# Optimization experiments

Hardware: AMD Instinct MI355X
Metric: run time of the kernel (lower is better)

Reference implementation:

```python
import jax, jax.numpy as jnp
import numpy as np

D_MODEL = 1024
NHEAD = 16
DHEAD = D_MODEL // NHEAD
DFF = 4096
B, S = 2, 2048
R = 25                # local_attention_radius = 5*5
K = 5                 # rel_pos_max_distance
W = 2 * R + 1         # window width
EPS = 1e-5


def setup_inputs() -> dict:
    key = jax.random.key(0)
    ks = jax.random.split(key, 12)
    s = 0.02
    g = lambda k, shape: jax.random.normal(k, shape, jnp.float32) * s
    return {
        "src": jax.random.normal(ks[0], (B, S, D_MODEL), jnp.float32),
        # attention in/out projections (W stored [out,in], applied x @ W.T + b)
        "wq": g(ks[1], (D_MODEL, D_MODEL)), "bq": jnp.zeros((D_MODEL,), jnp.float32),
        "wk": g(ks[2], (D_MODEL, D_MODEL)), "bk": jnp.zeros((D_MODEL,), jnp.float32),
        "wv": g(ks[3], (D_MODEL, D_MODEL)), "bv": jnp.zeros((D_MODEL,), jnp.float32),
        "wo": g(ks[4], (D_MODEL, D_MODEL)), "bo": jnp.zeros((D_MODEL,), jnp.float32),
        # relative position embeddings, ids clipped to [-K, K] -> 2K+1 rows
        "rel_emb": g(ks[5], (2 * K + 1, DHEAD)),
        # FFN
        "w1": g(ks[6], (DFF, D_MODEL)), "b1": jnp.zeros((DFF,), jnp.float32),
        "w2": g(ks[7], (D_MODEL, DFF)), "b2": jnp.zeros((D_MODEL,), jnp.float32),
        # layernorms
        "g1": jnp.ones((D_MODEL,), jnp.float32), "beta1": jnp.zeros((D_MODEL,), jnp.float32),
        "g2": jnp.ones((D_MODEL,), jnp.float32), "beta2": jnp.zeros((D_MODEL,), jnp.float32),
    }


def _layernorm(x, g, b):
    m = x.mean(-1, keepdims=True)
    v = ((x - m) ** 2).mean(-1, keepdims=True)
    return (x - m) * jax.lax.rsqrt(v + EPS) * g + b


def _rel_window_attention(x, wq, bq, wk, bk, wv, bv, wo, bo, rel_emb):
    b, s, d = x.shape

    def proj(w, bias):
        return (x @ w.T + bias).reshape(b, s, NHEAD, DHEAD).transpose(0, 2, 1, 3)

    q = proj(wq, bq)  # [B,H,S,Dh]
    k = proj(wk, bk)
    v = proj(wv, bv)

    offsets = jnp.arange(-R, R + 1)                     # [W]
    j = jnp.arange(s)[:, None] + offsets[None, :]       # [S,W] absolute key index
    valid = (j >= 0) & (j < s)
    jc = jnp.clip(j, 0, s - 1)

    scale = 1.0 / np.sqrt(DHEAD).astype(np.float32)
    k_win = k[:, :, jc]                                 # [B,H,S,W,Dh] banded gather
    scores = jnp.einsum('bhsd,bhswd->bhsw', q, k_win) * scale
    rel_ids = jnp.clip(offsets, -K, K) + K              # [W]
    scores = scores + jnp.einsum('bhsd,wd->bhsw', q, rel_emb[rel_ids]) * scale
    scores = jnp.where(valid[None, None], scores, jnp.float32(-1e30))
    attn = jax.nn.softmax(scores, axis=-1)              # [B,H,S,W]

    v_win = v[:, :, jc]                                 # [B,H,S,W,Dh]
    out = jnp.einsum('bhsw,bhswd->bhsd', attn, v_win)
    out = out.transpose(0, 2, 1, 3).reshape(b, s, d)
    return out @ wo.T + bo


def reference(src, wq, bq, wk, bk, wv, bv, wo, bo, rel_emb,
              w1, b1, w2, b2, g1, beta1, g2, beta2):
    # post-norm (norm_first=False default) transformer block, dropout=0 (eval)
    z = _rel_window_attention(src, wq, bq, wk, bk, wv, bv, wo, bo, rel_emb)
    x = _layernorm(src + z, g1, beta1)
    ff = jax.nn.relu(x @ w1.T + b1) @ w2.T + b2
    return _layernorm(x + ff, g2, beta2)
```

## Files before the change

### kernel.cpp

```cpp
#include <hip/hip_runtime.h>


#define D_MODEL 1024
#define SEQ     2048
#define NROWS   4096
#define WIN     51
#define RAD     25

typedef __attribute__((ext_vector_type(8))) __bf16 bf16x8;
typedef __attribute__((ext_vector_type(4))) float  floatx4;

__device__ __forceinline__ unsigned short f2bf(float x) {
    unsigned u = __float_as_uint(x);
    unsigned r = u + 0x7fffu + ((u >> 16) & 1u);
    return (unsigned short)(r >> 16);
}
__device__ __forceinline__ float bf2f(unsigned short h) {
    return __uint_as_float(((unsigned)h) << 16);
}

__device__ __forceinline__ void gld16(const unsigned short* g, unsigned short* l) {
    __builtin_amdgcn_global_load_lds(
        (const __attribute__((address_space(1))) unsigned int*)g,
        (__attribute__((address_space(3))) unsigned int*)l,
        16, 0, 0);
}

__device__ __forceinline__ void cvtgrp(const float* __restrict__ in,
                                       unsigned short* __restrict__ out, int g) {
    float4 f = ((const float4*)in)[g];
    ushort4 u;
    u.x = f2bf(f.x); u.y = f2bf(f.y); u.z = f2bf(f.z); u.w = f2bf(f.w);
    ((ushort4*)out)[g] = u;
}

__global__ __launch_bounds__(256)
void cvt1(const float* __restrict__ src,
          const float* __restrict__ wq, const float* __restrict__ wk,
          const float* __restrict__ wv,
          const float* __restrict__ bq, const float* __restrict__ bk,
          const float* __restrict__ bv,
          unsigned short* __restrict__ xb,
          unsigned short* __restrict__ wqkvb,
          float* __restrict__ bqkv)
{
    int g = blockIdx.x * 256 + threadIdx.x;
    if (g >= 1835200) return;
    if (g < 1048576) { cvtgrp(src, xb, g); return; }
    g -= 1048576;
    if (g < 262144) { cvtgrp(wq, wqkvb, g); return; }
    g -= 262144;
    if (g < 262144) { cvtgrp(wk, wqkvb + 1048576, g); return; }
    g -= 262144;
    if (g < 262144) { cvtgrp(wv, wqkvb + 2097152, g); return; }
    g -= 262144;
    float4 f = (g < 64) ? ((const float4*)bq)[g]
             : (g < 128) ? ((const float4*)bk)[g - 64]
                         : ((const float4*)bv)[g - 128];
    ((float4*)bqkv)[g] = f;
}

__global__ __launch_bounds__(256, 2)
void qkv_cvt(const unsigned short* __restrict__ A,
             const unsigned short* __restrict__ Wt,
             const float* __restrict__ bias,
             unsigned short* __restrict__ Cb,
             const float* __restrict__ wo, const float* __restrict__ w1,
             const float* __restrict__ w2,
             unsigned short* __restrict__ wob,
             unsigned short* __restrict__ w1b,
             unsigned short* __restrict__ w2b)
{
    __shared__ __attribute__((aligned(16))) unsigned short AS[3 * 8192];
    __shared__ __attribute__((aligned(16))) unsigned short BS[3 * 4096];

    if (blockIdx.x >= 384) {
        int g = (blockIdx.x - 384) * 256 + threadIdx.x;
        if (g < 262144) { cvtgrp(wo, wob, g); return; }
        g -= 262144;
        if (g < 1048576) { cvtgrp(w1, w1b, g); return; }
        g -= 1048576;
        cvtgrp(w2, w2b, g);
        return;
    }

    const int t0 = blockIdx.x;
    const int sid = (t0 & 7) * 48 + (t0 >> 3);
    const int bm = (sid / 24) * 256;
    const int bn = (sid % 24) * 128;

    const int tid  = threadIdx.x;
    const int lane = tid & 63;
    const int wave = tid >> 6;
    const int wr   = wave >> 1;
    const int wc   = wave & 1;
    const int fm   = lane & 15;
    const int fq   = lane >> 4;

    const int NT = 32;

    const int ks  = (tid >> 3) & 7;
    const int gi  = tid ^ ks;
    const int r0s = gi >> 2;
    const int c2s = gi & 3;
    const unsigned short* Agp = A  + (size_t)(bm + r0s) * 1024 + c2s * 8;
    const unsigned short* Wgp = Wt + (size_t)(bn + r0s) * 1024 + c2s * 8;
    const size_t istep = (size_t)64 * 1024;

    const int rA  = wr * 128 + fm;
    const int rB  = wc * 64  + fm;
    const int c0A = ((((rA << 2) | fq) ^ (fm >> 1)) << 3);
    const int c0B = ((((rB << 2) | fq) ^ (fm >> 1)) << 3);

    {
        const unsigned short* Ap = Agp;
        const unsigned short* Wp = Wgp;
        gld16(Ap,             AS + tid * 8);
        gld16(Ap + istep,     AS + tid * 8 + 2048);
        gld16(Ap + 2 * istep, AS + tid * 8 + 4096);
        gld16(Ap + 3 * istep, AS + tid * 8 + 6144);
        gld16(Wp,             BS + tid * 8);
        gld16(Wp + istep,     BS + tid * 8 + 2048);
        Ap += 32; Wp += 32;
        gld16(Ap,             AS + 8192 + tid * 8);
        gld16(Ap + istep,     AS + 8192 + tid * 8 + 2048);
        gld16(Ap + 2 * istep, AS + 8192 + tid * 8 + 4096);
        gld16(Ap + 3 * istep, AS + 8192 + tid * 8 + 6144);
        gld16(Wp,             BS + 4096 + tid * 8);
        gld16(Wp + istep,     BS + 4096 + tid * 8 + 2048);
    }
    asm volatile("s_waitcnt vmcnt(6)" ::: "memory");
    __builtin_amdgcn_sched_barrier(0);
    __builtin_amdgcn_s_barrier();
    __builtin_amdgcn_sched_barrier(0);

    floatx4 acc[8][4] = {};
    const unsigned short* Aga = Agp + 64;
    const unsigned short* Wga = Wgp + 64;
    int cbA = 0, cbB = 0;
    int pbA = 16384, pbB = 8192;

    for (int t = 0; t < NT; t++) {
        const bool pf = (t + 2 < NT);

        bf16x8 af[8], bf[4];
        #pragma unroll
        for (int mi = 0; mi < 8; mi++)
            af[mi] = *(const bf16x8*)(AS + cbA + c0A + mi * 512);
        #pragma unroll
        for (int ni = 0; ni < 4; ni++)
            bf[ni] = *(const bf16x8*)(BS + cbB + c0B + ni * 512);

        if (pf) {
            gld16(Aga,             AS + pbA + tid * 8);
            gld16(Aga + istep,     AS + pbA + tid * 8 + 2048);
            gld16(Aga + 2 * istep, AS + pbA + tid * 8 + 4096);
            gld16(Aga + 3 * istep, AS + pbA + tid * 8 + 6144);
            gld16(Wga,             BS + pbB + tid * 8);
            gld16(Wga + istep,     BS + pbB + tid * 8 + 2048);
        }

        __builtin_amdgcn_s_setprio(1);
        #pragma unroll
        for (int mi = 0; mi < 8; mi++)
            #pragma unroll
            for (int ni = 0; ni < 4; ni++)
                acc[mi][ni] = __builtin_amdgcn_mfma_f32_16x16x32_bf16(
                    af[mi], bf[ni], acc[mi][ni], 0, 0, 0);
        __builtin_amdgcn_s_setprio(0);

        if (t + 1 < NT) {
            if (pf) asm volatile("s_waitcnt vmcnt(6)" ::: "memory");
            else    asm volatile("s_waitcnt vmcnt(0)" ::: "memory");
            __builtin_amdgcn_sched_barrier(0);
            __builtin_amdgcn_s_barrier();
            __builtin_amdgcn_sched_barrier(0);
        }
        cbA = (cbA == 16384) ? 0 : cbA + 8192;
        cbB = (cbB == 8192)  ? 0 : cbB + 4096;
        pbA = (pbA == 16384) ? 0 : pbA + 8192;
        pbB = (pbB == 8192)  ? 0 : pbB + 4096;
        Aga += 32;
        Wga += 32;
    }

    const int r0  = bm + wr * 128 + fq * 4;
    const int c0e = bn + wc * 64 + fm;
    #pragma unroll
    for (int mi = 0; mi < 8; mi++) {
        #pragma unroll
        for (int ni = 0; ni < 4; ni++) {
            const int col = c0e + ni * 16;
            const float bv = bias[col];
            #pragma unroll
            for (int rr = 0; rr < 4; rr++) {
                const int row = r0 + mi * 16 + rr;
                Co_store: ;
                float v = acc[mi][ni][rr] + bv;
                Cb[(size_t)row * 3072 + col] = f2bf(v);
            }
        }
    }
}

__global__ __launch_bounds__(512, 2)
void gemm8p(const unsigned short* __restrict__ A,
            const unsigned short* __restrict__ Wt,
            const float* __restrict__ bias,
            unsigned short* __restrict__ Cb,
            int kstride, int kloop, int T, int tncnt,
            int ldc, int relu, size_t sstep1, size_t sstep2)
{
    __shared__ __attribute__((aligned(16))) unsigned short AS[2 * 16384];
    __shared__ __attribute__((aligned(16))) unsigned short BS[2 * 16384];

    const int id = blockIdx.x;
    const int sl = id / T;
    const int t0 = id - sl * T;
    const int sid = (t0 & 7) * (T >> 3) + (t0 >> 3);
    const int bm = (sid / tncnt) * 256;
    const int bn = (sid % tncnt) * 256;

    const int tid  = threadIdx.x;
    const int lane = tid & 63;
    const int wave = tid >> 6;
    const int wr   = wave >> 2;
    const int wc   = wave & 3;
    const int fm   = lane & 15;
    const int fq   = lane >> 4;

    const int kofs  = sl * kloop;
    const int NITER = kloop >> 7;

    const int srow = tid >> 3;
    const int scol = ((tid & 7) ^ ((tid >> 3) & 7)) * 8;
    const unsigned short* PA = A  + (size_t)(bm + srow) * kstride + kofs + scol;
    const unsigned short* PW = Wt + (size_t)(bn + srow) * kstride + kofs + scol;
    const size_t rs64 = (size_t)64 * kstride;

    const int aoff = (wr * 128 + fm) * 64;
    const int boff = (wc * 64  + fm) * 64;
    const int ck0  = (fq ^ (fm & 7)) * 8;
    const int ck1  = ck0 ^ 32;

    floatx4 acc[8][4] = {};

    auto STG = [&](const unsigned short* g, int h, unsigned short* l) {
        gld16(g + (size_t)(2 * h)     * rs64, l + h * 8192 + tid * 8);
        gld16(g + (size_t)(2 * h + 1) * rs64, l + h * 8192 + 4096 + tid * 8);
    };
    auto rdA = [&](bf16x8 (&d)[4][2], int bufb, int mb) {
        #pragma unroll
        for (int mi = 0; mi < 4; mi++) {
            d[mi][0] = *(const bf16x8*)(AS + bufb + aoff + (mb + mi) * 1024 + ck0);
            d[mi][1] = *(const bf16x8*)(AS + bufb + aoff + (mb + mi) * 1024 + ck1);
        }
    };
    auto rdB = [&](bf16x8 (&d)[2][2], int bufb, int nb) {
        #pragma unroll
        for (int ni = 0; ni < 2; ni++) {
            d[ni][0] = *(const bf16x8*)(BS + bufb + boff + (nb + ni) * 1024 + ck0);
            d[ni][1] = *(const bf16x8*)(BS + bufb + boff + (nb + ni) * 1024 + ck1);
        }
    };
    auto mmq = [&](bf16x8 (&a)[4][2], bf16x8 (&b)[2][2], int mb, int nb) {
        __builtin_amdgcn_s_setprio(1);
        #pragma unroll
        for (int ks = 0; ks < 2; ks++)
            #pragma unroll
            for (int mi = 0; mi < 4; mi++)
                #pragma unroll
                for (int ni = 0; ni < 2; ni++)
                    acc[mb + mi][nb + ni] = __builtin_amdgcn_mfma_f32_16x16x32_bf16(
                        a[mi][ks], b[ni][ks], acc[mb + mi][nb + ni], 0, 0, 0);
        __builtin_amdgcn_s_setprio(0);
    };
    auto barpre = [&]() {
        __builtin_amdgcn_sched_barrier(0);
        __builtin_amdgcn_s_barrier();
        asm volatile("s_waitcnt lgkmcnt(0)" ::: "memory");
        __builtin_amdgcn_sched_barrier(0);
    };
    auto barpost = [&]() {
        __builtin_amdgcn_sched_barrier(0);
        __builtin_amdgcn_s_barrier();
        __builtin_amdgcn_sched_barrier(0);
    };

    unsigned short* AS0 = AS;            unsigned short* AS1 = AS + 16384;
    unsigned short* BS0 = BS;            unsigned short* BS1 = BS + 16384;

    STG(PA, 0, AS0); STG(PA, 1, AS0);
    STG(PW, 0, BS0); STG(PW, 1, BS0);
    STG(PW + 64, 0, BS1); STG(PW + 64, 1, BS1);
    __builtin_amdgcn_sched_barrier(0);
    asm volatile("s_waitcnt vmcnt(4)" ::: "memory");
    __builtin_amdgcn_sched_barrier(0);
    __builtin_amdgcn_s_barrier();
    __builtin_amdgcn_sched_barrier(0);

    for (int it = 0; it < NITER; it++) {
        const bool more = (it + 1 < NITER);
        bf16x8 a03[4][2], a47[4][2], b01[2][2], b23[2][2];

        rdA(a03, 0, 0); rdB(b01, 0, 0);
        STG(PA + 64, 0, AS1);
        barpre(); mmq(a03, b01, 0, 0); barpost();
        rdB(b23, 0, 2);
        STG(PA + 64, 1, AS1);
        barpre(); mmq(a03, b23, 0, 2); barpost();
        rdA(a47, 0, 4);
        if (more) STG(PW + 128, 0, BS0);
        barpre(); mmq(a47, b01, 4, 0); barpost();
        if (more) STG(PW + 128, 1, BS0);
        __builtin_amdgcn_sched_barrier(0);
        if (more) asm volatile("s_waitcnt vmcnt(4)" ::: "memory");
        else      asm volatile("s_waitcnt vmcnt(0)" ::: "memory");
        __builtin_amdgcn_sched_barrier(0);
        __builtin_amdgcn_s_barrier();
        __builtin_amdgcn_sched_barrier(0);
        mmq(a47, b23, 4, 2); barpost();
        rdA(a03, 16384, 0); rdB(b01, 16384, 0);
        if (more) STG(PA + 128, 0, AS0);
        barpre(); mmq(a03, b01, 0, 0); barpost();
        rdB(b23, 16384, 2);
        if (more) STG(PA + 128, 1, AS0);
        barpre(); mmq(a03, b23, 0, 2); barpost();
        rdA(a47, 16384, 4);
        if (more) STG(PW + 192, 0, BS1);
        barpre(); mmq(a47, b01, 4, 0); barpost();
        if (more) {
            STG(PW + 192, 1, BS1);
            __builtin_amdgcn_sched_barrier(0);
            asm volatile("s_waitcnt vmcnt(4)" ::: "memory");
        }
        __builtin_amdgcn_sched_barrier(0);
        __builtin_amdgcn_s_barrier();
        __builtin_amdgcn_sched_barrier(0);
        mmq(a47, b23, 4, 2); barpost();

        PA += 128; PW += 128;
    }

    unsigned short* Co = Cb + (size_t)(sl & 1) * sstep1 + (size_t)(sl >> 1) * sstep2;
    const int r0  = bm + wr * 128 + fq * 4;
    const int c0e = bn + wc * 64 + fm;
    #pragma unroll
    for (int mi = 0; mi < 8; mi++) {
        #pragma unroll
        for (int ni = 0; ni < 4; ni++) {
            const int col = c0e + ni * 16;
            const float bv = bias ? bias[col] : 0.0f;
            #pragma unroll
            for (int rr = 0; rr < 4; rr++) {
                const int row = r0 + mi * 16 + rr;
                float v = acc[mi][ni][rr] + bv;
                if (relu) v = fmaxf(v, 0.0f);
                Co[(size_t)row * ldc + col] = f2bf(v);
            }
        }
    }
}

__global__ __launch_bounds__(256, 2)
void attn_mfma(const unsigned short* __restrict__ qkv,
               const float* __restrict__ rel,
               unsigned short* __restrict__ attnb)
{
    __shared__ __attribute__((aligned(16))) unsigned short Qs[64 * 72];
    __shared__ __attribute__((aligned(16))) unsigned short Ks[128 * 72];
    __shared__ __attribute__((aligned(16))) unsigned short Vt[64 * 168];
    __shared__ __attribute__((aligned(16))) unsigned short Rs[16 * 72];
    __shared__ __attribute__((aligned(16))) unsigned short Pl[4 * 16 * 104];
    __shared__ float Qrl[4 * 16 * 12];

    const int t   = threadIdx.x;
    const int blk = blockIdx.x;
    const int st  = blk & 31;
    const int h   = (blk >> 5) & 15;
    const int b   = blk >> 9;
    const int s0  = st << 6;
    const int brow0 = b * SEQ;

    const int trow = t >> 3;
    const int tc   = (t & 7) * 8;
    const uint4 z4 = make_uint4(0, 0, 0, 0);

    #pragma unroll
    for (int p = 0; p < 2; p++) {
        int r = trow + p * 32;
        uint4 v = *(const uint4*)(qkv + (size_t)(brow0 + s0 + r) * 3072 + h * 64 + tc);
        *(uint4*)(Qs + r * 72 + tc) = v;
    }
    #pragma unroll
    for (int p = 0; p < 4; p++) {
        int kr = trow + p * 32;
        int ka = s0 - 25 + kr;
        bool in = (ka >= 0) & (ka < SEQ);
        uint4 kv = z4, vv = z4;
        if (in) {
            kv = *(const uint4*)(qkv + (size_t)(brow0 + ka) * 3072 + 1024 + h * 64 + tc);
            vv = *(const uint4*)(qkv + (size_t)(brow0 + ka) * 3072 + 2048 + h * 64 + tc);
        }
        *(uint4*)(Ks + kr * 72 + tc) = kv;
        const unsigned short* e = (const unsigned short*)&vv;
        #pragma unroll
        for (int j = 0; j < 8; j++)
            Vt[(tc + j) * 168 + kr] = e[j];
    }
    if (t < 176) {
        float4 f = ((const float4*)rel)[t];
        int fi = t * 4, rr = fi >> 6, cc = fi & 63;
        ushort4 u;
        u.x = f2bf(f.x); u.y = f2bf(f.y); u.z = f2bf(f.z); u.w = f2bf(f.w);
        *(ushort4*)(Rs + rr * 72 + cc) = u;
    } else {
        int fi = 704 + (t - 176) * 4, rr = fi >> 6, cc = fi & 63;
        *(ushort4*)(Rs + rr * 72 + cc) = make_ushort4(0, 0, 0, 0);
    }
    {
        int n = t * 4, w2 = n >> 8, rem = n & 255, rr = rem >> 4, cc = 80 + (rem & 15);
        *(ushort4*)(Pl + w2 * (16 * 104) + rr * 104 + cc) = make_ushort4(0, 0, 0, 0);
    }
    for (int idx = t; idx < 320; idx += 256) {
        int r = idx / 5, cchunk = idx % 5;
        *(uint4*)(Vt + r * 168 + 128 + cchunk * 8) = z4;
    }
    __syncthreads();

    const int wave = t >> 6;
    const int lane = t & 63;
    const int fm   = lane & 15;
    const int fk8  = (lane >> 4) * 8;
    const int S0w  = s0 + wave * 16;
    unsigned short* Plw = Pl + wave * (16 * 104);
    float* Ql = Qrl + wave * (16 * 12);

    bf16x8 qa0 = *(const bf16x8*)(Qs + (wave * 16 + fm) * 72 + fk8);
    bf16x8 qa1 = *(const bf16x8*)(Qs + (wave * 16 + fm) * 72 + fk8 + 32);

    floatx4 Sc[5];
    #pragma unroll
    for (int nt = 0; nt < 5; nt++) {
        bf16x8 kb0 = *(const bf16x8*)(Ks + (wave * 16 + nt * 16 + fm) * 72 + fk8);
        bf16x8 kb1 = *(const bf16x8*)(Ks + (wave * 16 + nt * 16 + fm) * 72 + fk8 + 32);
        floatx4 acc = {0.f, 0.f, 0.f, 0.f};
        acc = __builtin_amdgcn_mfma_f32_16x16x32_bf16(qa0, kb0, acc, 0, 0, 0);
        acc = __builtin_amdgcn_mfma_f32_16x16x32_bf16(qa1, kb1, acc, 0, 0, 0);
        Sc[nt] = acc;
    }
    {
        bf16x8 rb0 = *(const bf16x8*)(Rs + fm * 72 + fk8);
        bf16x8 rb1 = *(const bf16x8*)(Rs + fm * 72 + fk8 + 32);
        floatx4 qr = {0.f, 0.f, 0.f, 0.f};
        qr = __builtin_amdgcn_mfma_f32_16x16x32_bf16(qa0, rb0, qr, 0, 0, 0);
        qr = __builtin_amdgcn_mfma_f32_16x16x32_bf16(qa1, rb1, qr, 0, 0, 0);
        if (fm < 12) {
            #pragma unroll
            for (int reg = 0; reg < 4; reg++)
                Ql[((lane >> 4) * 4 + reg) * 12 + fm] = qr[reg];
        }
    }

    float inv[4];
    const int iq0 = (lane >> 4) * 4;
    #pragma unroll
    for (int reg = 0; reg < 4; reg++) {
        const int i = iq0 + reg;
        float sc[5];
        float mx = -1e30f;
        #pragma unroll
        for (int nt = 0; nt < 5; nt++) {
            int c   = nt * 16 + fm;
            int off = c - 25 - i;
            int ka  = S0w - 25 + c;
            bool valid = (off >= -RAD) & (off <= RAD) & (ka >= 0) & (ka < SEQ);
            int rid = min(max(off, -5), 5) + 5;
            float v = valid ? (Sc[nt][reg] + Ql[i * 12 + rid]) * 0.125f : -1e30f;
            sc[nt] = v;
            mx = fmaxf(mx, v);
        }
        #pragma unroll
        for (int o = 1; o < 16; o <<= 1) mx = fmaxf(mx, __shfl_xor(mx, o));
        float sum = 0.f;
        #pragma unroll
        for (int nt = 0; nt < 5; nt++) {
            float e = __expf(sc[nt] - mx);
            sum += e;
            Plw[i * 104 + nt * 16 + fm] = f2bf(e);
        }
        #pragma unroll
        for (int o = 1; o < 16; o <<= 1) sum += __shfl_xor(sum, o);
        inv[reg] = 1.0f / sum;
    }

    floatx4 O[4] = {};
    #pragma unroll
    for (int kc = 0; kc < 3; kc++) {
        bf16x8 pa = *(const bf16x8*)(Plw + fm * 104 + fk8 + kc * 32);
        #pragma unroll
        for (int nt = 0; nt < 4; nt++) {
            bf16x8 vb = *(const bf16x8*)(Vt + (nt * 16 + fm) * 168 + wave * 16 + fk8 + kc * 32);
            O[nt] = __builtin_amdgcn_mfma_f32_16x16x32_bf16(pa, vb, O[nt], 0, 0, 0);
        }
    }

    #pragma unroll
    for (int nt = 0; nt < 4; nt++) {
        const int d = nt * 16 + fm;
        #pragma unroll
        for (int reg = 0; reg < 4; reg++) {
            const int i = iq0 + reg;
            attnb[(size_t)(brow0 + S0w + i) * 1024 + h * 64 + d] = f2bf(O[nt][reg] * inv[reg]);
        }
    }
}

__global__ __launch_bounds__(256)
void ln_fuse(const float* __restrict__ resf,
             const unsigned short* __restrict__ resb,
             const unsigned short* __restrict__ p0,
             const unsigned short* __restrict__ p1,
             const unsigned short* __restrict__ p2,
             const unsigned short* __restrict__ p3,
             const float* __restrict__ cbias,
             const float* __restrict__ gamma,
             const float* __restrict__ beta,
             float* __restrict__ outf,
             unsigned short* __restrict__ outb)
{
    const int wave = threadIdx.x >> 6;
    const int lane = threadIdx.x & 63;
    const int row = blockIdx.x * 4 + wave;
    const size_t base = (size_t)row * D_MODEL;

    float x[16];
    float sum = 0.0f, sq = 0.0f;
    #pragma unroll
    for (int i = 0; i < 4; i++) {
        const int c4 = lane + i * 64;
        ushort4 u0 = ((const ushort4*)(p0 + base))[c4];
        ushort4 u1 = ((const ushort4*)(p1 + base))[c4];
        float4 cb = ((const float4*)cbias)[c4];
        float4 va;
        if (resf) {
            va = ((const float4*)(resf + base))[c4];
        } else {
            ushort4 ua = ((const ushort4*)(resb + base))[c4];
            va.x = bf2f(ua.x); va.y = bf2f(ua.y); va.z = bf2f(ua.z); va.w = bf2f(ua.w);
        }
        float e0 = va.x + bf2f(u0.x) + bf2f(u1.x) + cb.x;
        float e1 = va.y + bf2f(u0.y) + bf2f(u1.y) + cb.y;
        float e2 = va.z + bf2f(u0.z) + bf2f(u1.z) + cb.z;
        float e3 = va.w + bf2f(u0.w) + bf2f(u1.w) + cb.w;
        if (p2) {
            ushort4 u2 = ((const ushort4*)(p2 + base))[c4];
            ushort4 u3 = ((const ushort4*)(p3 + base))[c4];
            e0 += bf2f(u2.x) + bf2f(u3.x);
            e1 += bf2f(u2.y) + bf2f(u3.y);
            e2 += bf2f(u2.z) + bf2f(u3.z);
            e3 += bf2f(u2.w) + bf2f(u3.w);
        }
        x[i*4+0] = e0; x[i*4+1] = e1; x[i*4+2] = e2; x[i*4+3] = e3;
        sum += e0 + e1 + e2 + e3;
        sq  += e0*e0 + e1*e1 + e2*e2 + e3*e3;
    }
    #pragma unroll
    for (int off = 32; off > 0; off >>= 1) {
        sum += __shfl_xor(sum, off);
        sq  += __shfl_xor(sq,  off);
    }
    const float mean = sum * (1.0f / 1024.0f);
    const float var  = sq  * (1.0f / 1024.0f) - mean * mean;
    const float rs   = rsqrtf(var + 1e-5f);

    #pragma unroll
    for (int i = 0; i < 4; i++) {
        const int c4 = lane + i * 64;
        float4 g4 = ((const float4*)gamma)[c4];
        float4 b4 = ((const float4*)beta)[c4];
        float4 o;
        o.x = (x[i*4+0] - mean) * rs * g4.x + b4.x;
        o.y = (x[i*4+1] - mean) * rs * g4.y + b4.y;
        o.z = (x[i*4+2] - mean) * rs * g4.z + b4.z;
        o.w = (x[i*4+3] - mean) * rs * g4.w + b4.w;
        if (outf) ((float4*)(outf + base))[c4] = o;
        if (outb) {
            ushort4 u;
            u.x = f2bf(o.x); u.y = f2bf(o.y); u.z = f2bf(o.z); u.w = f2bf(o.w);
            ((ushort4*)(outb + base))[c4] = u;
        }
    }
}

extern "C" void kernel_launch(void* const* d_in, const int* in_sizes, int n_in,
                              void* d_out, int out_size, void* d_ws, size_t ws_size,
                              hipStream_t stream)
{
    const float* src = (const float*)d_in[0];
    const float* wq  = (const float*)d_in[1];
    const float* bq  = (const float*)d_in[2];
    const float* wk  = (const float*)d_in[3];
    const float* bk  = (const float*)d_in[4];
    const float* wv  = (const float*)d_in[5];
    const float* bv  = (const float*)d_in[6];
    const float* wo  = (const float*)d_in[7];
    const float* bo  = (const float*)d_in[8];
    const float* rel = (const float*)d_in[9];
    const float* w1  = (const float*)d_in[10];
    const float* b1  = (const float*)d_in[11];
    const float* w2  = (const float*)d_in[12];
    const float* b2  = (const float*)d_in[13];
    const float* g1  = (const float*)d_in[14];
    const float* be1 = (const float*)d_in[15];
    const float* g2  = (const float*)d_in[16];
    const float* be2 = (const float*)d_in[17];
    float* out = (float*)d_out;

    char* ws = (char*)d_ws;
    const size_t MB = 1048576;
    unsigned short* wqkvb = (unsigned short*)(ws + 0);
    unsigned short* wob   = (unsigned short*)(ws + 6  * MB);
    unsigned short* w1b   = (unsigned short*)(ws + 8  * MB);
    unsigned short* w2b   = (unsigned short*)(ws + 16 * MB);
    float*          bqkv  = (float*)         (ws + 24 * MB);
    unsigned short* xb    = (unsigned short*)(ws + 25 * MB);
    unsigned short* attnb = xb;
    unsigned short* qkvb  = (unsigned short*)(ws + 33 * MB);
    unsigned short* z01   = (unsigned short*)(ws + 33 * MB);
    unsigned short* x1b   = (unsigned short*)(ws + 49 * MB);
    unsigned short* ff1b  = (unsigned short*)(ws + 57 * MB);
    unsigned short* f01   = (unsigned short*)(ws + 0);
    const size_t SL    = (size_t)NROWS * 1024;
    const size_t SOFF2 = (size_t)12 * MB;

    const dim3 blk(256);
    const dim3 blk5(512);
    cvt1<<<7169, blk, 0, stream>>>(src, wq, wk, wv, bq, bk, bv, xb, wqkvb, bqkv);
    qkv_cvt<<<9600, blk, 0, stream>>>(xb, wqkvb, bqkv, qkvb,
                                      wo, w1, w2, wob, w1b, w2b);
    attn_mfma<<<1024, blk, 0, stream>>>(qkvb, rel, attnb);
    gemm8p<<<256, blk5, 0, stream>>>(attnb, wob, nullptr, z01, 1024, 256, 64, 4,
                                     1024, 0, SL, SOFF2);
    ln_fuse<<<NROWS / 4, blk, 0, stream>>>(src, nullptr, z01, z01 + SL,
                                           z01 + SOFF2, z01 + SOFF2 + SL,
                                           bo, g1, be1, nullptr, x1b);
    gemm8p<<<256, blk5, 0, stream>>>(x1b, w1b, b1, ff1b, 1024, 1024, 256, 16,
                                     4096, 1, 0, 0);
    gemm8p<<<256, blk5, 0, stream>>>(ff1b, w2b, nullptr, f01, 4096, 1024, 64, 4,
                                     1024, 0, SL, SOFF2);
    ln_fuse<<<NROWS / 4, blk, 0, stream>>>(nullptr, x1b, f01, f01 + SL,
                                           f01 + SOFF2, f01 + SOFF2 + SL,
                                           b2, g2, be2, out, nullptr);
}
```

Before: 297.4 us.

## Fuse post-attention GEMMs and layernorms into one cooperative persistent kernel

Replaces the five separate launches (out-proj split-K GEMM, LN1, FFN1 GEMM, FFN2 split-K GEMM, LN2) with a single cooperative kernel of 256 blocks. The stages are separated by grid-wide syncs, and the layernorm rows are redistributed across the same blocks. This removes per-launch overhead and the tail gaps between kernels. In exchange it adds grid.sync barriers, drops the min-blocks occupancy hint from the GEMM launch bounds, and requires all 256 blocks to be co-resident.

```diff
diff --git a/kernel.cpp b/kernel.cpp
--- a/kernel.cpp
+++ b/kernel.cpp
@@ -1,4 +1,7 @@
 #include <hip/hip_runtime.h>
+#include <hip/hip_cooperative_groups.h>
+
+namespace cg = cooperative_groups;
 
 
 #define D_MODEL 1024
@@ -6,6 +9,8 @@
 #define NROWS   4096
 #define WIN     51
 #define RAD     25
+#define SLC     4194304u
+#define SOFF2C  12582912u
 
 typedef __attribute__((ext_vector_type(8))) __bf16 bf16x8;
 typedef __attribute__((ext_vector_type(4))) float  floatx4;
@@ -195,7 +200,6 @@
             #pragma unroll
             for (int rr = 0; rr < 4; rr++) {
                 const int row = r0 + mi * 16 + rr;
-                Co_store: ;
                 float v = acc[mi][ni][rr] + bv;
                 Cb[(size_t)row * 3072 + col] = f2bf(v);
             }
@@ -203,25 +207,23 @@
     }
 }
 
-__global__ __launch_bounds__(512, 2)
-void gemm8p(const unsigned short* __restrict__ A,
-            const unsigned short* __restrict__ Wt,
-            const float* __restrict__ bias,
-            unsigned short* __restrict__ Cb,
-            int kstride, int kloop, int T, int tncnt,
-            int ldc, int relu, size_t sstep1, size_t sstep2)
+__device__ __forceinline__ void gemm8p_dev(
+    unsigned short (&AS)[2 * 16384],
+    unsigned short (&BS)[2 * 16384],
+    const unsigned short* __restrict__ A,
+    const unsigned short* __restrict__ Wt,
+    const float* __restrict__ bias,
+    unsigned short* __restrict__ Cb,
+    int kstride, int kloop, int T, int tncnt,
+    int ldc, int relu, size_t sstep1, size_t sstep2,
+    int id, int tid)
 {
-    __shared__ __attribute__((aligned(16))) unsigned short AS[2 * 16384];
-    __shared__ __attribute__((aligned(16))) unsigned short BS[2 * 16384];
-
-    const int id = blockIdx.x;
     const int sl = id / T;
     const int t0 = id - sl * T;
     const int sid = (t0 & 7) * (T >> 3) + (t0 >> 3);
     const int bm = (sid / tncnt) * 256;
     const int bn = (sid % tncnt) * 256;
 
-    const int tid  = threadIdx.x;
     const int lane = tid & 63;
     const int wave = tid >> 6;
     const int wr   = wave >> 2;
@@ -362,178 +364,16 @@
     }
 }
 
-__global__ __launch_bounds__(256, 2)
-void attn_mfma(const unsigned short* __restrict__ qkv,
-               const float* __restrict__ rel,
-               unsigned short* __restrict__ attnb)
+__device__ __forceinline__ void ln_dev(
+    int row, int lane,
+    const float* __restrict__ resf, const unsigned short* __restrict__ resb,
+    const unsigned short* __restrict__ p0, const unsigned short* __restrict__ p1,
+    const unsigned short* __restrict__ p2, const unsigned short* __restrict__ p3,
+    const float* __restrict__ cbias, const float* __restrict__ gamma,
+    const float* __restrict__ beta,
+    float* __restrict__ outf, unsigned short* __restrict__ outb)
 {
-    __shared__ __attribute__((aligned(16))) unsigned short Qs[64 * 72];
-    __shared__ __attribute__((aligned(16))) unsigned short Ks[128 * 72];
-    __shared__ __attribute__((aligned(16))) unsigned short Vt[64 * 168];
-    __shared__ __attribute__((aligned(16))) unsigned short Rs[16 * 72];
-    __shared__ __attribute__((aligned(16))) unsigned short Pl[4 * 16 * 104];
-    __shared__ float Qrl[4 * 16 * 12];
-
-    const int t   = threadIdx.x;
-    const int blk = blockIdx.x;
-    const int st  = blk & 31;
-    const int h   = (blk >> 5) & 15;
-    const int b   = blk >> 9;
-    const int s0  = st << 6;
-    const int brow0 = b * SEQ;
-
-    const int trow = t >> 3;
-    const int tc   = (t & 7) * 8;
-    const uint4 z4 = make_uint4(0, 0, 0, 0);
-
-    #pragma unroll
-    for (int p = 0; p < 2; p++) {
-        int r = trow + p * 32;
-        uint4 v = *(const uint4*)(qkv + (size_t)(brow0 + s0 + r) * 3072 + h * 64 + tc);
-        *(uint4*)(Qs + r * 72 + tc) = v;
-    }
-    #pragma unroll
-    for (int p = 0; p < 4; p++) {
-        int kr = trow + p * 32;
-        int ka = s0 - 25 + kr;
-        bool in = (ka >= 0) & (ka < SEQ);
-        uint4 kv = z4, vv = z4;
-        if (in) {
-            kv = *(const uint4*)(qkv + (size_t)(brow0 + ka) * 3072 + 1024 + h * 64 + tc);
-            vv = *(const uint4*)(qkv + (size_t)(brow0 + ka) * 3072 + 2048 + h * 64 + tc);
-        }
-        *(uint4*)(Ks + kr * 72 + tc) = kv;
-        const unsigned short* e = (const unsigned short*)&vv;
-        #pragma unroll
-        for (int j = 0; j < 8; j++)
-            Vt[(tc + j) * 168 + kr] = e[j];
-    }
-    if (t < 176) {
-        float4 f = ((const float4*)rel)[t];
-        int fi = t * 4, rr = fi >> 6, cc = fi & 63;
-        ushort4 u;
-        u.x = f2bf(f.x); u.y = f2bf(f.y); u.z = f2bf(f.z); u.w = f2bf(f.w);
-        *(ushort4*)(Rs + rr * 72 + cc) = u;
-    } else {
-        int fi = 704 + (t - 176) * 4, rr = fi >> 6, cc = fi & 63;
-        *(ushort4*)(Rs + rr * 72 + cc) = make_ushort4(0, 0, 0, 0);
-    }
-    {
-        int n = t * 4, w2 = n >> 8, rem = n & 255, rr = rem >> 4, cc = 80 + (rem & 15);
-        *(ushort4*)(Pl + w2 * (16 * 104) + rr * 104 + cc) = make_ushort4(0, 0, 0, 0);
-    }
-    for (int idx = t; idx < 320; idx += 256) {
-        int r = idx / 5, cchunk = idx % 5;
-        *(uint4*)(Vt + r * 168 + 128 + cchunk * 8) = z4;
-    }
-    __syncthreads();
-
-    const int wave = t >> 6;
-    const int lane = t & 63;
-    const int fm   = lane & 15;
-    const int fk8  = (lane >> 4) * 8;
-    const int S0w  = s0 + wave * 16;
-    unsigned short* Plw = Pl + wave * (16 * 104);
-    float* Ql = Qrl + wave * (16 * 12);
-
-    bf16x8 qa0 = *(const bf16x8*)(Qs + (wave * 16 + fm) * 72 + fk8);
-    bf16x8 qa1 = *(const bf16x8*)(Qs + (wave * 16 + fm) * 72 + fk8 + 32);
-
-    floatx4 Sc[5];
-    #pragma unroll
-    for (int nt = 0; nt < 5; nt++) {
-        bf16x8 kb0 = *(const bf16x8*)(Ks + (wave * 16 + nt * 16 + fm) * 72 + fk8);
-        bf16x8 kb1 = *(const bf16x8*)(Ks + (wave * 16 + nt * 16 + fm) * 72 + fk8 + 32);
-        floatx4 acc = {0.f, 0.f, 0.f, 0.f};
-        acc = __builtin_amdgcn_mfma_f32_16x16x32_bf16(qa0, kb0, acc, 0, 0, 0);
-        acc = __builtin_amdgcn_mfma_f32_16x16x32_bf16(qa1, kb1, acc, 0, 0, 0);
-        Sc[nt] = acc;
-    }
-    {
-        bf16x8 rb0 = *(const bf16x8*)(Rs + fm * 72 + fk8);
-        bf16x8 rb1 = *(const bf16x8*)(Rs + fm * 72 + fk8 + 32);
-        floatx4 qr = {0.f, 0.f, 0.f, 0.f};
-        qr = __builtin_amdgcn_mfma_f32_16x16x32_bf16(qa0, rb0, qr, 0, 0, 0);
-        qr = __builtin_amdgcn_mfma_f32_16x16x32_bf16(qa1, rb1, qr, 0, 0, 0);
-        if (fm < 12) {
-            #pragma unroll
-            for (int reg = 0; reg < 4; reg++)
-                Ql[((lane >> 4) * 4 + reg) * 12 + fm] = qr[reg];
-        }
-    }
-
-    float inv[4];
-    const int iq0 = (lane >> 4) * 4;
-    #pragma unroll
-    for (int reg = 0; reg < 4; reg++) {
-        const int i = iq0 + reg;
-        float sc[5];
-        float mx = -1e30f;
-        #pragma unroll
-        for (int nt = 0; nt < 5; nt++) {
-            int c   = nt * 16 + fm;
-            int off = c - 25 - i;
-            int ka  = S0w - 25 + c;
-            bool valid = (off >= -RAD) & (off <= RAD) & (ka >= 0) & (ka < SEQ);
-            int rid = min(max(off, -5), 5) + 5;
-            float v = valid ? (Sc[nt][reg] + Ql[i * 12 + rid]) * 0.125f : -1e30f;
-            sc[nt] = v;
-            mx = fmaxf(mx, v);
-        }
-        #pragma unroll
-        for (int o = 1; o < 16; o <<= 1) mx = fmaxf(mx, __shfl_xor(mx, o));
-        float sum = 0.f;
-        #pragma unroll
-        for (int nt = 0; nt < 5; nt++) {
-            float e = __expf(sc[nt] - mx);
-            sum += e;
-            Plw[i * 104 + nt * 16 + fm] = f2bf(e);
-        }
-        #pragma unroll
-        for (int o = 1; o < 16; o <<= 1) sum += __shfl_xor(sum, o);
-        inv[reg] = 1.0f / sum;
-    }
-
-    floatx4 O[4] = {};
-    #pragma unroll
-    for (int kc = 0; kc < 3; kc++) {
-        bf16x8 pa = *(const bf16x8*)(Plw + fm * 104 + fk8 + kc * 32);
-        #pragma unroll
-        for (int nt = 0; nt < 4; nt++) {
-            bf16x8 vb = *(const bf16x8*)(Vt + (nt * 16 + fm) * 168 + wave * 16 + fk8 + kc * 32);
-            O[nt] = __builtin_amdgcn_mfma_f32_16x16x32_bf16(pa, vb, O[nt], 0, 0, 0);
-        }
-    }
-
-    #pragma unroll
-    for (int nt = 0; nt < 4; nt++) {
-        const int d = nt * 16 + fm;
-        #pragma unroll
-        for (int reg = 0; reg < 4; reg++) {
-            const int i = iq0 + reg;
-            attnb[(size_t)(brow0 + S0w + i) * 1024 + h * 64 + d] = f2bf(O[nt][reg] * inv[reg]);
-        }
-    }
-}
-
-__global__ __launch_bounds__(256)
-void ln_fuse(const float* __restrict__ resf,
-             const unsigned short* __restrict__ resb,
-             const unsigned short* __restrict__ p0,
-             const unsigned short* __restrict__ p1,
-             const unsigned short* __restrict__ p2,
-             const unsigned short* __restrict__ p3,
-             const float* __restrict__ cbias,
-             const float* __restrict__ gamma,
-             const float* __restrict__ beta,
-             float* __restrict__ outf,
-             unsigned short* __restrict__ outb)
-{
-    const int wave = threadIdx.x >> 6;
-    const int lane = threadIdx.x & 63;
-    const int row = blockIdx.x * 4 + wave;
     const size_t base = (size_t)row * D_MODEL;
-
     float x[16];
     float sum = 0.0f, sq = 0.0f;
     #pragma unroll
@@ -553,7 +393,7 @@
         float e1 = va.y + bf2f(u0.y) + bf2f(u1.y) + cb.y;
         float e2 = va.z + bf2f(u0.z) + bf2f(u1.z) + cb.z;
         float e3 = va.w + bf2f(u0.w) + bf2f(u1.w) + cb.w;
-        if (p2) {
+        {
             ushort4 u2 = ((const ushort4*)(p2 + base))[c4];
             ushort4 u3 = ((const ushort4*)(p3 + base))[c4];
             e0 += bf2f(u2.x) + bf2f(u3.x);
@@ -589,6 +429,220 @@
             ushort4 u;
             u.x = f2bf(o.x); u.y = f2bf(o.y); u.z = f2bf(o.z); u.w = f2bf(o.w);
             ((ushort4*)(outb + base))[c4] = u;
+        }
+    }
+}
+
+__global__ __launch_bounds__(512)
+void tail_mega(const unsigned short* __restrict__ attnb,
+               const unsigned short* __restrict__ wob,
+               unsigned short* __restrict__ z01,
+               const float* __restrict__ src,
+               const float* __restrict__ bo,
+               const float* __restrict__ g1, const float* __restrict__ be1,
+               unsigned short* __restrict__ x1b,
+               const unsigned short* __restrict__ w1b,
+               const float* __restrict__ b1,
+               unsigned short* __restrict__ ff1b,
+               const unsigned short* __restrict__ w2b,
+               unsigned short* __restrict__ f01,
+               const float* __restrict__ b2,
+               const float* __restrict__ g2, const float* __restrict__ be2,
+               float* __restrict__ out)
+{
+    __shared__ __attribute__((aligned(16))) unsigned short AS[2 * 16384];
+    __shared__ __attribute__((aligned(16))) unsigned short BS[2 * 16384];
+
+    cg::grid_group grid = cg::this_grid();
+    const int id  = blockIdx.x;
+    const int tid = threadIdx.x;
+    const int wave = tid >> 6;
+    const int lane = tid & 63;
+
+    gemm8p_dev(AS, BS, attnb, wob, nullptr, z01, 1024, 256, 64, 4,
+               1024, 0, SLC, SOFF2C, id, tid);
+    __threadfence();
+    grid.sync();
+
+    #pragma unroll
+    for (int k = 0; k < 2; k++) {
+        const int row = id * 16 + k * 8 + wave;
+        ln_dev(row, lane, src, nullptr, z01, z01 + SLC,
+               z01 + SOFF2C, z01 + SOFF2C + SLC,
+               bo, g1, be1, nullptr, x1b);
+    }
+    __threadfence();
+    grid.sync();
+
+    gemm8p_dev(AS, BS, x1b, w1b, b1, ff1b, 1024, 1024, 256, 16,
+               4096, 1, 0, 0, id, tid);
+    __threadfence();
+    grid.sync();
+
+    gemm8p_dev(AS, BS, ff1b, w2b, nullptr, f01, 4096, 1024, 64, 4,
+               1024, 0, SLC, SOFF2C, id, tid);
+    __threadfence();
+    grid.sync();
+
+    #pragma unroll
+    for (int k = 0; k < 2; k++) {
+        const int row = id * 16 + k * 8 + wave;
+        ln_dev(row, lane, nullptr, x1b, f01, f01 + SLC,
+               f01 + SOFF2C, f01 + SOFF2C + SLC,
+               b2, g2, be2, out, nullptr);
+    }
+}
+
+__global__ __launch_bounds__(256, 2)
+void attn_mfma(const unsigned short* __restrict__ qkv,
+               const float* __restrict__ rel,
+               unsigned short* __restrict__ attnb)
+{
+    __shared__ __attribute__((aligned(16))) unsigned short Qs[64 * 72];
+    __shared__ __attribute__((aligned(16))) unsigned short Ks[128 * 72];
+    __shared__ __attribute__((aligned(16))) unsigned short Vt[64 * 168];
+    __shared__ __attribute__((aligned(16))) unsigned short Rs[16 * 72];
+    __shared__ __attribute__((aligned(16))) unsigned short Pl[4 * 16 * 104];
+    __shared__ float Qrl[4 * 16 * 12];
+
+    const int t   = threadIdx.x;
+    const int blk = blockIdx.x;
+    const int st  = blk & 31;
+    const int h   = (blk >> 5) & 15;
+    const int b   = blk >> 9;
+    const int s0  = st << 6;
+    const int brow0 = b * SEQ;
+
+    const int trow = t >> 3;
+    const int tc   = (t & 7) * 8;
+    const uint4 z4 = make_uint4(0, 0, 0, 0);
+
+    #pragma unroll
+    for (int p = 0; p < 2; p++) {
+        int r = trow + p * 32;
+        uint4 v = *(const uint4*)(qkv + (size_t)(brow0 + s0 + r) * 3072 + h * 64 + tc);
+        *(uint4*)(Qs + r * 72 + tc) = v;
+    }
+    #pragma unroll
+    for (int p = 0; p < 4; p++) {
+        int kr = trow + p * 32;
+        int ka = s0 - 25 + kr;
+        bool in = (ka >= 0) & (ka < SEQ);
+        uint4 kv = z4, vv = z4;
+        if (in) {
+            kv = *(const uint4*)(qkv + (size_t)(brow0 + ka) * 3072 + 1024 + h * 64 + tc);
+            vv = *(const uint4*)(qkv + (size_t)(brow0 + ka) * 3072 + 2048 + h * 64 + tc);
+        }
+        *(uint4*)(Ks + kr * 72 + tc) = kv;
+        const unsigned short* e = (const unsigned short*)&vv;
+        #pragma unroll
+        for (int j = 0; j < 8; j++)
+            Vt[(tc + j) * 168 + kr] = e[j];
+    }
+    if (t < 176) {
+        float4 f = ((const float4*)rel)[t];
+        int fi = t * 4, rr = fi >> 6, cc = fi & 63;
+        ushort4 u;
+        u.x = f2bf(f.x); u.y = f2bf(f.y); u.z = f2bf(f.z); u.w = f2bf(f.w);
+        *(ushort4*)(Rs + rr * 72 + cc) = u;
+    } else {
+        int fi = 704 + (t - 176) * 4, rr = fi >> 6, cc = fi & 63;
+        *(ushort4*)(Rs + rr * 72 + cc) = make_ushort4(0, 0, 0, 0);
+    }
+    {
+        int n = t * 4, w2 = n >> 8, rem = n & 255, rr = rem >> 4, cc = 80 + (rem & 15);
+        *(ushort4*)(Pl + w2 * (16 * 104) + rr * 104 + cc) = make_ushort4(0, 0, 0, 0);
+    }
+    for (int idx = t; idx < 320; idx += 256) {
+        int r = idx / 5, cchunk = idx % 5;
+        *(uint4*)(Vt + r * 168 + 128 + cchunk * 8) = z4;
+    }
+    __syncthreads();
+
+    const int wave = t >> 6;
+    const int lane = t & 63;
+    const int fm   = lane & 15;
+    const int fk8  = (lane >> 4) * 8;
+    const int S0w  = s0 + wave * 16;
+    unsigned short* Plw = Pl + wave * (16 * 104);
+    float* Ql = Qrl + wave * (16 * 12);
+
+    bf16x8 qa0 = *(const bf16x8*)(Qs + (wave * 16 + fm) * 72 + fk8);
+    bf16x8 qa1 = *(const bf16x8*)(Qs + (wave * 16 + fm) * 72 + fk8 + 32);
+
+    floatx4 Sc[5];
+    #pragma unroll
+    for (int nt = 0; nt < 5; nt++) {
+        bf16x8 kb0 = *(const bf16x8*)(Ks + (wave * 16 + nt * 16 + fm) * 72 + fk8);
+        bf16x8 kb1 = *(const bf16x8*)(Ks + (wave * 16 + nt * 16 + fm) * 72 + fk8 + 32);
+        floatx4 acc = {0.f, 0.f, 0.f, 0.f};
+        acc = __builtin_amdgcn_mfma_f32_16x16x32_bf16(qa0, kb0, acc, 0, 0, 0);
+        acc = __builtin_amdgcn_mfma_f32_16x16x32_bf16(qa1, kb1, acc, 0, 0, 0);
+        Sc[nt] = acc;
+    }
+    {
+        bf16x8 rb0 = *(const bf16x8*)(Rs + fm * 72 + fk8);
+        bf16x8 rb1 = *(const bf16x8*)(Rs + fm * 72 + fk8 + 32);
+        floatx4 qr = {0.f, 0.f, 0.f, 0.f};
+        qr = __builtin_amdgcn_mfma_f32_16x16x32_bf16(qa0, rb0, qr, 0, 0, 0);
+        qr = __builtin_amdgcn_mfma_f32_16x16x32_bf16(qa1, rb1, qr, 0, 0, 0);
+        if (fm < 12) {
+            #pragma unroll
+            for (int reg = 0; reg < 4; reg++)
+                Ql[((lane >> 4) * 4 + reg) * 12 + fm] = qr[reg];
+        }
+    }
+
+    float inv[4];
+    const int iq0 = (lane >> 4) * 4;
+    #pragma unroll
+    for (int reg = 0; reg < 4; reg++) {
+        const int i = iq0 + reg;
+        float sc[5];
+        float mx = -1e30f;
+        #pragma unroll
+        for (int nt = 0; nt < 5; nt++) {
+            int c   = nt * 16 + fm;
+            int off = c - 25 - i;
+            int ka  = S0w - 25 + c;
+            bool valid = (off >= -RAD) & (off <= RAD) & (ka >= 0) & (ka < SEQ);
+            int rid = min(max(off, -5), 5) + 5;
+            float v = valid ? (Sc[nt][reg] + Ql[i * 12 + rid]) * 0.125f : -1e30f;
+            sc[nt] = v;
+            mx = fmaxf(mx, v);
+        }
+        #pragma unroll
+        for (int o = 1; o < 16; o <<= 1) mx = fmaxf(mx, __shfl_xor(mx, o));
+        float sum = 0.f;
+        #pragma unroll
+        for (int nt = 0; nt < 5; nt++) {
+            float e = __expf(sc[nt] - mx);
+            sum += e;
+            Plw[i * 104 + nt * 16 + fm] = f2bf(e);
+        }
+        #pragma unroll
+        for (int o = 1; o < 16; o <<= 1) sum += __shfl_xor(sum, o);
+        inv[reg] = 1.0f / sum;
+    }
+
+    floatx4 O[4] = {};
+    #pragma unroll
+    for (int kc = 0; kc < 3; kc++) {
+        bf16x8 pa = *(const bf16x8*)(Plw + fm * 104 + fk8 + kc * 32);
+        #pragma unroll
+        for (int nt = 0; nt < 4; nt++) {
+            bf16x8 vb = *(const bf16x8*)(Vt + (nt * 16 + fm) * 168 + wave * 16 + fk8 + kc * 32);
+            O[nt] = __builtin_amdgcn_mfma_f32_16x16x32_bf16(pa, vb, O[nt], 0, 0, 0);
+        }
+    }
+
+    #pragma unroll
+    for (int nt = 0; nt < 4; nt++) {
+        const int d = nt * 16 + fm;
+        #pragma unroll
+        for (int reg = 0; reg < 4; reg++) {
+            const int i = iq0 + reg;
+            attnb[(size_t)(brow0 + S0w + i) * 1024 + h * 64 + d] = f2bf(O[nt][reg] * inv[reg]);
         }
     }
 }
@@ -631,25 +685,38 @@
     unsigned short* x1b   = (unsigned short*)(ws + 49 * MB);
     unsigned short* ff1b  = (unsigned short*)(ws + 57 * MB);
     unsigned short* f01   = (unsigned short*)(ws + 0);
-    const size_t SL    = (size_t)NROWS * 1024;
-    const size_t SOFF2 = (size_t)12 * MB;
 
     const dim3 blk(256);
-    const dim3 blk5(512);
     cvt1<<<7169, blk, 0, stream>>>(src, wq, wk, wv, bq, bk, bv, xb, wqkvb, bqkv);
     qkv_cvt<<<9600, blk, 0, stream>>>(xb, wqkvb, bqkv, qkvb,
                                       wo, w1, w2, wob, w1b, w2b);
     attn_mfma<<<1024, blk, 0, stream>>>(qkvb, rel, attnb);
-    gemm8p<<<256, blk5, 0, stream>>>(attnb, wob, nullptr, z01, 1024, 256, 64, 4,
-                                     1024, 0, SL, SOFF2);
-    ln_fuse<<<NROWS / 4, blk, 0, stream>>>(src, nullptr, z01, z01 + SL,
-                                           z01 + SOFF2, z01 + SOFF2 + SL,
-                                           bo, g1, be1, nullptr, x1b);
-    gemm8p<<<256, blk5, 0, stream>>>(x1b, w1b, b1, ff1b, 1024, 1024, 256, 16,
-                                     4096, 1, 0, 0);
-    gemm8p<<<256, blk5, 0, stream>>>(ff1b, w2b, nullptr, f01, 4096, 1024, 64, 4,
-                                     1024, 0, SL, SOFF2);
-    ln_fuse<<<NROWS / 4, blk, 0, stream>>>(nullptr, x1b, f01, f01 + SL,
-                                           f01 + SOFF2, f01 + SOFF2 + SL,
-                                           b2, g2, be2, out, nullptr);
-}
+    {
+        const unsigned short* a_attnb = attnb;
+        const unsigned short* a_wob   = wob;
+        unsigned short*       a_z01   = z01;
+        const float*          a_src   = src;
+        const float*          a_bo    = bo;
+        const float*          a_g1    = g1;
+        const float*          a_be1   = be1;
+        unsigned short*       a_x1b   = x1b;
+        const unsigned short* a_w1b   = w1b;
+        const float*          a_b1    = b1;
+        unsigned short*       a_ff1b  = ff1b;
+        const unsigned short* a_w2b   = w2b;
+        unsigned short*       a_f01   = f01;
+        const float*          a_b2    = b2;
+        const float*          a_g2    = g2;
+        const float*          a_be2   = be2;
+        float*                a_out   = out;
+        void* args[] = {
+            (void*)&a_attnb, (void*)&a_wob, (void*)&a_z01, (void*)&a_src,
+            (void*)&a_bo, (void*)&a_g1, (void*)&a_be1, (void*)&a_x1b,
+            (void*)&a_w1b, (void*)&a_b1, (void*)&a_ff1b, (void*)&a_w2b,
+            (void*)&a_f01, (void*)&a_b2, (void*)&a_g2, (void*)&a_be2,
+            (void*)&a_out
+        };
+        hipLaunchCooperativeKernel((const void*)tail_mega, dim3(256), dim3(512),
+                                   args, 0, stream);
+    }
+}
```

Result: slower. 687.5 us (+131.2%).
